# Kernel tuning notes

Hardware: AMD Instinct MI355X
Metric: run time of the kernel (lower is better)

## Reference

```python
import jax, jax.numpy as jnp
import numpy as np

# config: input_shape=(1024,1024), upsampling_scale=4, input_over_output_stride=4
OUT_H = 1024  # int(1024 * 4 / 4)
OUT_W = 1024
SCALE = 4.0 / 4.0  # upscale / stride


def setup_inputs() -> dict:
    key = jax.random.key(0)
    k1, k2 = jax.random.split(key)
    B, N = 128, 256
    # centers anywhere on the grid; wh in [20, 200) so most boxes have nonzero sigma
    boxes_center = jax.random.uniform(k1, (B, N, 2), jnp.float32) * jnp.array([OUT_W, OUT_H], jnp.float32)
    boxes_wh = jax.random.uniform(k2, (B, N, 2), jnp.float32) * 180.0 + 20.0
    return {"boxes_center": boxes_center, "boxes_wh": boxes_wh}


def _forward(boxes_center, boxes_wh):
    Wb = boxes_wh[..., 0]
    Hb = boxes_wh[..., 1]
    # kernel size = W//2*2 - 1 ; radius = (ks-1)//2 ; sigma = radius//3 (all floor-div, as numpy)
    ksw = jnp.floor(Wb / 2) * 2 - 1
    rw = jnp.floor((ksw - 1) / 2)
    sw = jnp.floor(rw / 3)
    ksh = jnp.floor(Hb / 2) * 2 - 1
    rh = jnp.floor((ksh - 1) / 2)
    sh = jnp.floor(rh / 3)

    zero_box = (boxes_center.sum(-1) + boxes_wh.sum(-1)) == 0

    # lmks = (lmks * upscale / stride).astype(int32): truncation toward zero
    x = jnp.trunc(boxes_center[..., 0] * SCALE)
    y = jnp.trunc(boxes_center[..., 1] * SCALE)

    ul0 = x - rw
    ul1 = y - rh
    br0 = x + rw + 1
    br1 = y + rh + 1

    def in_img(a, b):  # is_point_in_img: 0 <= a <= W and 0 <= b <= H (inclusive)
        return (a >= 0) & (a <= OUT_W) & (b >= 0) & (b <= OUT_H)

    active = (~zero_box) & (sw != 0) & (sh != 0) & (in_img(ul0, ul1) | in_img(br0, br1))  # [B,N]

    def splat(center, sig, lo, hi, n):
        # at grid position p, written value = exp(-(p - center)^2 / (2*sigma^2))
        # for p in [max(0, lo), min(n, hi)), since kernel center aligns with `center`.
        p = jnp.arange(n, dtype=jnp.float32)  # [n]
        safe = jnp.where(sig == 0, 1.0, sig)
        g = jnp.exp(-((p - center[..., None]) ** 2) / (2.0 * safe[..., None] ** 2))  # [B,N,n]
        m = (p >= lo[..., None]) & (p < hi[..., None]) & active[..., None]
        return jnp.where(m, g, 0.0)

    vector_x = splat(x, sw, ul0, br0, OUT_W)  # [B,N,OUT_W]
    vector_y = splat(y, sh, ul1, br1, OUT_H)  # [B,N,OUT_H]
    return vector_x, vector_y


def reference(boxes_center, boxes_wh):
    return _forward(boxes_center, boxes_wh)
```

## Files before the change

### kernel.cpp

```cpp
#include <hip/hip_runtime.h>

#define OUT_W 1024
#define OUT_H 1024

__global__ __launch_bounds__(256)
void gv_kernel(const float* __restrict__ center,
               const float* __restrict__ wh,
               float* __restrict__ out_x,
               float* __restrict__ out_y)
{
    const int bn = blockIdx.x;
    const int t  = threadIdx.x;

    const float cx = center[2 * bn + 0];
    const float cy = center[2 * bn + 1];
    const float Wb = wh[2 * bn + 0];
    const float Hb = wh[2 * bn + 1];

    const float ksw = floorf(Wb * 0.5f) * 2.0f - 1.0f;
    const float rw  = floorf((ksw - 1.0f) * 0.5f);
    const float sw  = floorf(rw / 3.0f);
    const float ksh = floorf(Hb * 0.5f) * 2.0f - 1.0f;
    const float rh  = floorf((ksh - 1.0f) * 0.5f);
    const float sh  = floorf(rh / 3.0f);

    const bool zero_box = ((cx + cy) + (Wb + Hb)) == 0.0f;

    const float x = truncf(cx);
    const float y = truncf(cy);

    const float ul0 = x - rw;
    const float ul1 = y - rh;
    const float br0 = x + rw + 1.0f;
    const float br1 = y + rh + 1.0f;

    const bool in_ul = (ul0 >= 0.0f) && (ul0 <= (float)OUT_W) &&
                       (ul1 >= 0.0f) && (ul1 <= (float)OUT_H);
    const bool in_br = (br0 >= 0.0f) && (br0 <= (float)OUT_W) &&
                       (br1 >= 0.0f) && (br1 <= (float)OUT_H);
    const bool active = (!zero_box) && (sw != 0.0f) && (sh != 0.0f) && (in_ul || in_br);

    const float ssw = (sw == 0.0f) ? 1.0f : sw;
    const float ssh = (sh == 0.0f) ? 1.0f : sh;
    const float iw  = -1.0f / (2.0f * ssw * ssw);
    const float ih  = -1.0f / (2.0f * ssh * ssh);

    float rx[4], ry[4];
    const int p0 = t * 4;
#pragma unroll
    for (int i = 0; i < 4; ++i) {
        const float p  = (float)(p0 + i);
        const float dx = p - x;
        const float dy = p - y;
        const bool mx = active && (p >= ul0) && (p < br0);
        const bool my = active && (p >= ul1) && (p < br1);
        rx[i] = mx ? __expf(dx * dx * iw) : 0.0f;
        ry[i] = my ? __expf(dy * dy * ih) : 0.0f;
    }

    const size_t row = (size_t)bn * (OUT_W / 4) + t;
    reinterpret_cast<float4*>(out_x)[row] = make_float4(rx[0], rx[1], rx[2], rx[3]);
    reinterpret_cast<float4*>(out_y)[row] = make_float4(ry[0], ry[1], ry[2], ry[3]);
}

extern "C" void kernel_launch(void* const* d_in, const int* in_sizes, int n_in,
                              void* d_out, int out_size, void* d_ws, size_t ws_size,
                              hipStream_t stream) {
    const float* center = (const float*)d_in[0];
    const float* wh     = (const float*)d_in[1];
    float* out = (float*)d_out;

    const int BN = in_sizes[0] / 2;
    float* out_x = out;
    float* out_y = out + (size_t)BN * OUT_W;

    gv_kernel<<<dim3(BN), dim3(256), 0, stream>>>(center, wh, out_x, out_y);
}
```

Measured before the change: 252.5 us.

## Process eight boxes per block and use nontemporal vector stores

```diff
diff --git a/kernel.cpp b/kernel.cpp
--- a/kernel.cpp
+++ b/kernel.cpp
@@ -2,65 +2,87 @@
 
 #define OUT_W 1024
 #define OUT_H 1024
+#define BOXES 8
+
+typedef float floatx4 __attribute__((ext_vector_type(4)));
 
 __global__ __launch_bounds__(256)
 void gv_kernel(const float* __restrict__ center,
                const float* __restrict__ wh,
                float* __restrict__ out_x,
-               float* __restrict__ out_y)
+               float* __restrict__ out_y,
+               int BN)
 {
-    const int bn = blockIdx.x;
-    const int t  = threadIdx.x;
+    const int t    = threadIdx.x;
+    const int base = blockIdx.x * BOXES;
 
-    const float cx = center[2 * bn + 0];
-    const float cy = center[2 * bn + 1];
-    const float Wb = wh[2 * bn + 0];
-    const float Hb = wh[2 * bn + 1];
-
-    const float ksw = floorf(Wb * 0.5f) * 2.0f - 1.0f;
-    const float rw  = floorf((ksw - 1.0f) * 0.5f);
-    const float sw  = floorf(rw / 3.0f);
-    const float ksh = floorf(Hb * 0.5f) * 2.0f - 1.0f;
-    const float rh  = floorf((ksh - 1.0f) * 0.5f);
-    const float sh  = floorf(rh / 3.0f);
-
-    const bool zero_box = ((cx + cy) + (Wb + Hb)) == 0.0f;
-
-    const float x = truncf(cx);
-    const float y = truncf(cy);
-
-    const float ul0 = x - rw;
-    const float ul1 = y - rh;
-    const float br0 = x + rw + 1.0f;
-    const float br1 = y + rh + 1.0f;
-
-    const bool in_ul = (ul0 >= 0.0f) && (ul0 <= (float)OUT_W) &&
-                       (ul1 >= 0.0f) && (ul1 <= (float)OUT_H);
-    const bool in_br = (br0 >= 0.0f) && (br0 <= (float)OUT_W) &&
-                       (br1 >= 0.0f) && (br1 <= (float)OUT_H);
-    const bool active = (!zero_box) && (sw != 0.0f) && (sh != 0.0f) && (in_ul || in_br);
-
-    const float ssw = (sw == 0.0f) ? 1.0f : sw;
-    const float ssh = (sh == 0.0f) ? 1.0f : sh;
-    const float iw  = -1.0f / (2.0f * ssw * ssw);
-    const float ih  = -1.0f / (2.0f * ssh * ssh);
-
-    float rx[4], ry[4];
-    const int p0 = t * 4;
+    float cx[BOXES], cy[BOXES], Wb[BOXES], Hb[BOXES];
 #pragma unroll
-    for (int i = 0; i < 4; ++i) {
-        const float p  = (float)(p0 + i);
-        const float dx = p - x;
-        const float dy = p - y;
-        const bool mx = active && (p >= ul0) && (p < br0);
-        const bool my = active && (p >= ul1) && (p < br1);
-        rx[i] = mx ? __expf(dx * dx * iw) : 0.0f;
-        ry[i] = my ? __expf(dy * dy * ih) : 0.0f;
+    for (int j = 0; j < BOXES; ++j) {
+        const int bn = base + j;
+        if (bn < BN) {
+            const float2 c = reinterpret_cast<const float2*>(center)[bn];
+            const float2 w = reinterpret_cast<const float2*>(wh)[bn];
+            cx[j] = c.x; cy[j] = c.y; Wb[j] = w.x; Hb[j] = w.y;
+        } else {
+            cx[j] = 0.0f; cy[j] = 0.0f; Wb[j] = 0.0f; Hb[j] = 0.0f;
+        }
     }
 
-    const size_t row = (size_t)bn * (OUT_W / 4) + t;
-    reinterpret_cast<float4*>(out_x)[row] = make_float4(rx[0], rx[1], rx[2], rx[3]);
-    reinterpret_cast<float4*>(out_y)[row] = make_float4(ry[0], ry[1], ry[2], ry[3]);
+    const int   p0 = t * 4;
+    const float pf[4] = { (float)(p0 + 0), (float)(p0 + 1),
+                          (float)(p0 + 2), (float)(p0 + 3) };
+
+#pragma unroll
+    for (int j = 0; j < BOXES; ++j) {
+        const int bn = base + j;
+        if (bn >= BN) break;
+
+        const float ksw = floorf(Wb[j] * 0.5f) * 2.0f - 1.0f;
+        const float rw  = floorf((ksw - 1.0f) * 0.5f);
+        const float sw  = floorf(rw / 3.0f);
+        const float ksh = floorf(Hb[j] * 0.5f) * 2.0f - 1.0f;
+        const float rh  = floorf((ksh - 1.0f) * 0.5f);
+        const float sh  = floorf(rh / 3.0f);
+
+        const bool zero_box = ((cx[j] + cy[j]) + (Wb[j] + Hb[j])) == 0.0f;
+
+        const float x = truncf(cx[j]);
+        const float y = truncf(cy[j]);
+
+        const float ul0 = x - rw;
+        const float ul1 = y - rh;
+        const float br0 = x + rw + 1.0f;
+        const float br1 = y + rh + 1.0f;
+
+        const bool in_ul = (ul0 >= 0.0f) && (ul0 <= (float)OUT_W) &&
+                           (ul1 >= 0.0f) && (ul1 <= (float)OUT_H);
+        const bool in_br = (br0 >= 0.0f) && (br0 <= (float)OUT_W) &&
+                           (br1 >= 0.0f) && (br1 <= (float)OUT_H);
+        const bool active = (!zero_box) && (sw != 0.0f) && (sh != 0.0f) &&
+                            (in_ul || in_br);
+
+        const float ssw = (sw == 0.0f) ? 1.0f : sw;
+        const float ssh = (sh == 0.0f) ? 1.0f : sh;
+        const float iw  = -1.0f / (2.0f * ssw * ssw);
+        const float ih  = -1.0f / (2.0f * ssh * ssh);
+
+        floatx4 vx, vy;
+#pragma unroll
+        for (int i = 0; i < 4; ++i) {
+            const float p  = pf[i];
+            const float dx = p - x;
+            const float dy = p - y;
+            const bool mx = active && (p >= ul0) && (p < br0);
+            const bool my = active && (p >= ul1) && (p < br1);
+            vx[i] = mx ? __expf(dx * dx * iw) : 0.0f;
+            vy[i] = my ? __expf(dy * dy * ih) : 0.0f;
+        }
+
+        const size_t row = (size_t)bn * (OUT_W / 4) + t;
+        __builtin_nontemporal_store(vx, reinterpret_cast<floatx4*>(out_x) + row);
+        __builtin_nontemporal_store(vy, reinterpret_cast<floatx4*>(out_y) + row);
+    }
 }
 
 extern "C" void kernel_launch(void* const* d_in, const int* in_sizes, int n_in,
@@ -74,5 +96,6 @@
     float* out_x = out;
     float* out_y = out + (size_t)BN * OUT_W;
 
-    gv_kernel<<<dim3(BN), dim3(256), 0, stream>>>(center, wh, out_x, out_y);
+    const int grid = (BN + BOXES - 1) / BOXES;
+    gv_kernel<<<dim3(grid), dim3(256), 0, stream>>>(center, wh, out_x, out_y, BN);
 }
```

Result: slower. 269.6 us (+6.8%).

## Zero output with memset and splat only in-window elements, one wave per box

Applied to the files above, without the earlier changes.

```diff
diff --git a/kernel.cpp b/kernel.cpp
--- a/kernel.cpp
+++ b/kernel.cpp
@@ -4,18 +4,20 @@
 #define OUT_H 1024
 
 __global__ __launch_bounds__(256)
-void gv_kernel(const float* __restrict__ center,
-               const float* __restrict__ wh,
-               float* __restrict__ out_x,
-               float* __restrict__ out_y)
+void gv_splat(const float* __restrict__ center,
+              const float* __restrict__ wh,
+              float* __restrict__ out_x,
+              float* __restrict__ out_y,
+              int BN)
 {
-    const int bn = blockIdx.x;
-    const int t  = threadIdx.x;
+    const int wave = threadIdx.x >> 6;
+    const int lane = threadIdx.x & 63;
+    const int bn   = blockIdx.x * 4 + wave;
+    if (bn >= BN) return;
 
-    const float cx = center[2 * bn + 0];
-    const float cy = center[2 * bn + 1];
-    const float Wb = wh[2 * bn + 0];
-    const float Hb = wh[2 * bn + 1];
+    const float2 c = reinterpret_cast<const float2*>(center)[bn];
+    const float2 w = reinterpret_cast<const float2*>(wh)[bn];
+    const float cx = c.x, cy = c.y, Wb = w.x, Hb = w.y;
 
     const float ksw = floorf(Wb * 0.5f) * 2.0f - 1.0f;
     const float rw  = floorf((ksw - 1.0f) * 0.5f);
@@ -38,29 +40,29 @@
                        (ul1 >= 0.0f) && (ul1 <= (float)OUT_H);
     const bool in_br = (br0 >= 0.0f) && (br0 <= (float)OUT_W) &&
                        (br1 >= 0.0f) && (br1 <= (float)OUT_H);
-    const bool active = (!zero_box) && (sw != 0.0f) && (sh != 0.0f) && (in_ul || in_br);
+    const bool active = (!zero_box) && (sw != 0.0f) && (sh != 0.0f) &&
+                        (in_ul || in_br);
+    if (!active) return;
 
-    const float ssw = (sw == 0.0f) ? 1.0f : sw;
-    const float ssh = (sh == 0.0f) ? 1.0f : sh;
-    const float iw  = -1.0f / (2.0f * ssw * ssw);
-    const float ih  = -1.0f / (2.0f * ssh * ssh);
+    const float iw = -1.0f / (2.0f * sw * sw);
+    const float ih = -1.0f / (2.0f * sh * sh);
 
-    float rx[4], ry[4];
-    const int p0 = t * 4;
-#pragma unroll
-    for (int i = 0; i < 4; ++i) {
-        const float p  = (float)(p0 + i);
-        const float dx = p - x;
-        const float dy = p - y;
-        const bool mx = active && (p >= ul0) && (p < br0);
-        const bool my = active && (p >= ul1) && (p < br1);
-        rx[i] = mx ? __expf(dx * dx * iw) : 0.0f;
-        ry[i] = my ? __expf(dy * dy * ih) : 0.0f;
+    const int xs = max(0, (int)ul0);
+    const int xe = min(OUT_W, (int)br0);
+    const int ys = max(0, (int)ul1);
+    const int ye = min(OUT_H, (int)br1);
+
+    float* __restrict__ rowx = out_x + (size_t)bn * OUT_W;
+    float* __restrict__ rowy = out_y + (size_t)bn * OUT_W;
+
+    for (int p = xs + lane; p < xe; p += 64) {
+        const float dx = (float)p - x;
+        rowx[p] = __expf(dx * dx * iw);
     }
-
-    const size_t row = (size_t)bn * (OUT_W / 4) + t;
-    reinterpret_cast<float4*>(out_x)[row] = make_float4(rx[0], rx[1], rx[2], rx[3]);
-    reinterpret_cast<float4*>(out_y)[row] = make_float4(ry[0], ry[1], ry[2], ry[3]);
+    for (int p = ys + lane; p < ye; p += 64) {
+        const float dy = (float)p - y;
+        rowy[p] = __expf(dy * dy * ih);
+    }
 }
 
 extern "C" void kernel_launch(void* const* d_in, const int* in_sizes, int n_in,
@@ -74,5 +76,8 @@
     float* out_x = out;
     float* out_y = out + (size_t)BN * OUT_W;
 
-    gv_kernel<<<dim3(BN), dim3(256), 0, stream>>>(center, wh, out_x, out_y);
+    hipMemsetAsync(d_out, 0, (size_t)out_size, stream);
+
+    const int grid = (BN + 3) / 4;
+    gv_splat<<<dim3(grid), dim3(256), 0, stream>>>(center, wh, out_x, out_y, BN);
 }
```

Result: no change. 254.2 us (+0.7%).
